# Kernel optimization log

Measured on AMD Instinct MI355X. Metric: run time of the kernel, lower is better.

## Reference

```python
import jax, jax.numpy as jnp
import numpy as np

# ---- config mirroring init kwargs ----
D_MODEL = 512
NUM_DIRS = 8
QUANTILES = (0.1, 0.5, 0.9)
POLY_ORDER = 2
BETA_INIT = 0.5
HEAD_WIDTH = 16
SOFTSORT_C = 0.5
SOFTSORT_ALPHA = 0.5
FEAT_IN = NUM_DIRS * (len(QUANTILES) + POLY_ORDER + 1)  # 48


def _legendre_basis(T, order, dtype):
    t = jnp.linspace(-1.0, 1.0, T, dtype=dtype)
    P = [jnp.ones_like(t)]
    if order >= 1:
        P.append(t)
    for n in range(1, order):
        P.append(((2 * n + 1) * t * P[n] - n * P[n - 1]) / (n + 1))
    B = jnp.stack(P[:order + 1], axis=0)
    return B / jnp.sqrt(jnp.maximum(jnp.sum(B * B, axis=1, keepdims=True), 1e-6))


def _isotonic_nonincreasing(y):
    #   v_i = min_{s<=i} max_{t>=i} mean(y[s..t])
    T = y.shape[0]
    c = jnp.concatenate([jnp.zeros((1,), y.dtype), jnp.cumsum(y)])
    s_idx = jnp.arange(T)[:, None]
    t_idx = jnp.arange(T)[None, :]
    length = jnp.maximum(t_idx - s_idx + 1, 1).astype(y.dtype)
    A = (c[t_idx + 1] - c[s_idx]) / length                 # mean over [s, t]
    A = jnp.where(t_idx >= s_idx, A, -jnp.inf)
    R = jax.lax.cummax(A, axis=1, reverse=True)            # R[s,i] = max_{t>=i} A[s,t]
    R = jnp.where(s_idx <= t_idx, R, jnp.inf)
    V = jax.lax.cummin(R, axis=0)                          # V[i,i] = min_{s<=i} R[s,i]
    return jnp.diagonal(V)


def _soft_sort_ascending(vals, reg):
    # Blondel et al. fast-soft-sort with L2 regularization.
    # Descending soft-sort: rho/reg - isotonic_nonincreasing(rho/reg - sort_desc(theta))
    # Ascending = -soft_sort_desc(-vals).
    L, T = vals.shape
    theta = -vals
    s = jnp.sort(theta, axis=-1)[:, ::-1]                  # descending
    rho = jnp.arange(T, 0, -1, dtype=vals.dtype) / jnp.asarray(reg, vals.dtype)
    v = jax.vmap(_isotonic_nonincreasing)(rho[None, :] - s)
    return -(rho[None, :] - v)


def setup_inputs() -> dict:
    key = jax.random.key(0)
    ks = jax.random.split(key, 6)
    B, T, N, D = 2, 128, 128, D_MODEL
    x = jax.random.normal(ks[0], (B, T, N, D), dtype=jnp.float32)
    valid_mask = jnp.ones((B, T, N), dtype=jnp.float32)
    # proj: Linear(D, K, bias=False), kaiming-uniform-ish init
    bound = 1.0 / np.sqrt(D)
    W_proj = jax.random.uniform(ks[1], (NUM_DIRS, D), jnp.float32, -bound, bound)
    # additive head: per-feature Linear(1,width) -> GELU -> Linear(width,D,no bias)
    W1 = jax.random.uniform(ks[2], (FEAT_IN, HEAD_WIDTH), jnp.float32, -1.0, 1.0)
    b1 = jax.random.uniform(ks[3], (FEAT_IN, HEAD_WIDTH), jnp.float32, -1.0, 1.0)
    bw = 1.0 / np.sqrt(HEAD_WIDTH)
    W2 = jax.random.uniform(ks[4], (FEAT_IN, HEAD_WIDTH, D_MODEL), jnp.float32, -bw, bw)
    beta = jnp.full((D_MODEL,), BETA_INIT, dtype=jnp.float32)
    return {"x": x, "valid_mask": valid_mask, "W_proj": W_proj,
            "W1": W1, "b1": b1, "W2": W2, "beta": beta}


def reference(x, valid_mask, W_proj, W1, b1, W2, beta):
    B, T, N, D = x.shape
    K = W_proj.shape[0]
    # orthonormalize projection (done in-place under no_grad in torch -> straight-through)
    Q, _ = jnp.linalg.qr(W_proj.T)                          # [D, K]
    W_eff = W_proj + jax.lax.stop_gradient(Q.T - W_proj)
    U = W_eff.T                                             # [D, K]

    v = jnp.einsum('btnd,dk->btnk', x, U) * valid_mask[..., None]
    v_bnkt = jnp.transpose(v, (0, 2, 3, 1))                 # [B, N, K, T]

    reg = max(1e-3, SOFTSORT_C * float(T) ** (-SOFTSORT_ALPHA))
    ss = _soft_sort_ascending(v_bnkt.reshape(-1, T), reg)   # [L, T]

    levels = jnp.asarray(QUANTILES, x.dtype)
    pos = jnp.clip(levels, 0.0, 1.0) * (T - 1)
    lo = jnp.clip(jnp.floor(pos).astype(jnp.int32), 0, T - 1)
    hi = jnp.clip(jnp.ceil(pos).astype(jnp.int32), 0, T - 1)
    w = pos - lo.astype(x.dtype)
    qv = ((1.0 - w) * ss[:, lo] + w * ss[:, hi]).reshape(B, N, K, -1)

    Bmat = _legendre_basis(T, POLY_ORDER, x.dtype)          # [P+1, T]
    coeff = jnp.einsum('bnkt,pt->bnkp', v_bnkt, Bmat)

    feats = jnp.concatenate([qv, coeff], axis=-1).reshape(B, N, -1)  # [B, N, F]
    hmid = jax.nn.gelu(feats[..., None] * W1 + b1, approximate=False)  # [B, N, F, width]
    parts = jnp.einsum('bnfw,fwd->bnfd', hmid, W2)          # [B, N, F, D]
    y = parts.sum(axis=2)                                   # [B, N, D]

    beta_eff = jax.nn.sigmoid(beta)
    y_btnd = jnp.broadcast_to(y[:, None], (B, T, N, D))
    h = x + beta_eff * y_btnd
    vm = valid_mask[..., None]
    h = vm * h + (1.0 - vm) * x

    num = jnp.mean(jnp.sqrt(jnp.sum((beta_eff * y_btnd) ** 2, axis=-1)))
    den = jnp.maximum(jnp.mean(jnp.sqrt(jnp.sum(x * x, axis=-1))), 1e-9)
    r = jax.lax.stop_gradient(num / den)
    # per-feature energy: contributions are constant over T -> factor T inside sqrt
    sq = jnp.sum((beta_eff * parts) ** 2, axis=(1, 3))       # [B, F]
    energy = jnp.sqrt(jnp.asarray(T, x.dtype) * sq)
    r_feat = jax.lax.stop_gradient(jnp.mean(energy, axis=0) / den)
    return h, r, r_feat
```

## Files before the change

### kernel.cpp

```cpp
#include <hip/hip_runtime.h>
#include <hip/hip_bf16.h>
#include <math.h>

#define OFF_FEATS 5504
#define OFF_DENP  17792
#define OFF_NUMP  18816
#define OFF_SQP   19072
#define OFF_V     31360
#define OFF_Y     293504
#define OFF_YP    424576
#define WS_TOTAL  1473152

__device__ __align__(16) float g_ws[WS_TOTAL];

static __device__ __forceinline__ float wred64(float v){
  #pragma unroll
  for (int m = 32; m >= 1; m >>= 1) v += __shfl_xor(v, m, 64);
  return v;
}

__global__ __launch_bounds__(256) void k2_proj(const float* __restrict__ x,
                                               const float* __restrict__ vmask,
                                               const float* __restrict__ Wp){
  int tid = threadIdx.x;
  int l = tid & 63, wv = tid >> 6;
  int g = blockIdx.x*4 + wv;
  __shared__ float denw[4];
  float A[8][8], u[8][8], tau[8];
  #pragma unroll
  for (int c = 0; c < 8; c++)
    #pragma unroll
    for (int p = 0; p < 8; p++)
      A[c][p] = Wp[c*512 + l*8 + p];
  #pragma unroll
  for (int j = 0; j < 8; j++){
    float alpha = __shfl(A[j][j & 7], j >> 3, 64);
    float ssq = 0.0f;
    #pragma unroll
    for (int p = 0; p < 8; p++){
      int row = l*8 + p;
      float v = A[j][p];
      ssq += (row > j) ? v*v : 0.0f;
    }
    ssq = wred64(ssq);
    float tj, scale;
    if (ssq == 0.0f){ tj = 0.0f; scale = 0.0f; }
    else {
      float bta = -copysignf(sqrtf(alpha*alpha + ssq), alpha);
      tj = (bta - alpha)/bta;
      scale = 1.0f/(alpha - bta);
    }
    tau[j] = tj;
    #pragma unroll
    for (int p = 0; p < 8; p++){
      int row = l*8 + p;
      float v = A[j][p]*scale;
      A[j][p] = (row < j) ? 0.0f : (row == j ? 1.0f : v);
    }
    #pragma unroll
    for (int c = j+1; c < 8; c++){
      float d = 0.0f;
      #pragma unroll
      for (int p = 0; p < 8; p++) d += A[c][p]*A[j][p];
      d = wred64(d)*tj;
      #pragma unroll
      for (int p = 0; p < 8; p++) A[c][p] -= d*A[j][p];
    }
  }
  #pragma unroll
  for (int c = 0; c < 8; c++)
    #pragma unroll
    for (int p = 0; p < 8; p++)
      u[c][p] = (l*8 + p == c) ? 1.0f : 0.0f;
  #pragma unroll
  for (int j = 7; j >= 0; j--){
    #pragma unroll
    for (int c = 0; c < 8; c++){
      float d = 0.0f;
      #pragma unroll
      for (int p = 0; p < 8; p++) d += u[c][p]*A[j][p];
      d = wred64(d)*tau[j];
      #pragma unroll
      for (int p = 0; p < 8; p++) u[c][p] -= d*A[j][p];
    }
  }
  int kk = ((l & 1) << 2) | (l & 2) | ((l & 4) >> 2);
  float denpart = 0.0f;
  for (int rr = 0; rr < 8; rr++){
    int row = g*8 + rr;
    const float* xr = x + (size_t)row*512 + l*8;
    float4 xa = *(const float4*)xr;
    float4 xb = *(const float4*)(xr + 4);
    float xe[8] = {xa.x, xa.y, xa.z, xa.w, xb.x, xb.y, xb.z, xb.w};
    float acc[8];
    float sq = 0.0f;
    #pragma unroll
    for (int k = 0; k < 8; k++){
      float a = 0.0f;
      #pragma unroll
      for (int e = 0; e < 8; e++) a += xe[e]*u[k][e];
      acc[k] = a;
    }
    #pragma unroll
    for (int e = 0; e < 8; e++) sq += xe[e]*xe[e];
    if (l & 1){
      float t;
      t=acc[0];acc[0]=acc[4];acc[4]=t;
      t=acc[1];acc[1]=acc[5];acc[5]=t;
      t=acc[2];acc[2]=acc[6];acc[6]=t;
      t=acc[3];acc[3]=acc[7];acc[7]=t;
    }
    acc[0] += __shfl_xor(acc[4], 1, 64);
    acc[1] += __shfl_xor(acc[5], 1, 64);
    acc[2] += __shfl_xor(acc[6], 1, 64);
    acc[3] += __shfl_xor(acc[7], 1, 64);
    if (l & 2){
      float t;
      t=acc[0];acc[0]=acc[2];acc[2]=t;
      t=acc[1];acc[1]=acc[3];acc[3]=t;
    }
    acc[0] += __shfl_xor(acc[2], 2, 64);
    acc[1] += __shfl_xor(acc[3], 2, 64);
    if (l & 4){
      float t=acc[0];acc[0]=acc[1];acc[1]=t;
    }
    acc[0] += __shfl_xor(acc[1], 4, 64);
    acc[0] += __shfl_xor(acc[0], 8, 64);
    acc[0] += __shfl_xor(acc[0], 16, 64);
    acc[0] += __shfl_xor(acc[0], 32, 64);
    sq = wred64(sq);
    float vm = vmask[row];
    if (l < 8){
      int b = row >> 14, t = (row >> 7) & 127, n = row & 127;
      int bn = b*128 + n;
      g_ws[OFF_V + bn*1024 + kk*128 + t] = acc[0]*vm;
    }
    if (l == 0) denpart += sqrtf(sq);
  }
  if (l == 0) denw[wv] = denpart;
  __syncthreads();
  if (tid == 0) g_ws[OFF_DENP + blockIdx.x] = denw[0]+denw[1]+denw[2]+denw[3];
}

__global__ __launch_bounds__(256) void k3_sortfeat(){
  int tid = threadIdx.x;
  int l = tid & 63, wv = tid >> 6;
  int rho = blockIdx.x*4 + wv;
  __shared__ float orig[4][128], srt[4][128], Bl[384];
  __shared__ float pS[4][128];
  __shared__ int   pC[4][128];
  __shared__ float nrmS[2];
  if (tid < 128){
    float t = -1.0f + 2.0f*(float)tid/127.0f;
    Bl[128+tid] = t;
    Bl[256+tid] = 0.5f*(3.0f*t*t - 1.0f);
  }
  const float* vr = g_ws + OFF_V + rho*128;
  orig[wv][2*l]   = vr[2*l];
  orig[wv][2*l+1] = vr[2*l+1];
  srt[wv][2*l] = 0.0f; srt[wv][2*l+1] = 0.0f;
  __syncthreads();
  if (tid < 64){
    float a = Bl[128+tid]*Bl[128+tid] + Bl[192+tid]*Bl[192+tid];
    float b = Bl[256+tid]*Bl[256+tid] + Bl[320+tid]*Bl[320+tid];
    a = wred64(a); b = wred64(b);
    if (tid == 0){
      nrmS[0] = sqrtf(fmaxf(a, 1e-6f));
      nrmS[1] = sqrtf(fmaxf(b, 1e-6f));
    }
  }
  __syncthreads();
  if (tid < 128){
    Bl[tid] = 0.08838834764831845f;
    Bl[128+tid] /= nrmS[0];
    Bl[256+tid] /= nrmS[1];
  }
  __syncthreads();
  float c0, c1, c2;
  {
    float a = orig[wv][2*l], b = orig[wv][2*l+1];
    c0 = a*Bl[2*l]       + b*Bl[2*l+1];
    c1 = a*Bl[128+2*l]   + b*Bl[128+2*l+1];
    c2 = a*Bl[256+2*l]   + b*Bl[256+2*l+1];
  }
  c0 = wred64(c0); c1 = wred64(c1); c2 = wred64(c2);
  float e0 = orig[wv][2*l], e1 = orig[wv][2*l+1];
  int r0 = 0, r1 = 0;
  #pragma unroll 4
  for (int j = 0; j < 128; j++){
    float vj = orig[wv][j];
    r0 += (vj < e0) || (vj == e0 && j < 2*l);
    r1 += (vj < e1) || (vj == e1 && j < 2*l+1);
  }
  srt[wv][r0] = e0;
  srt[wv][r1] = e1;
  __syncthreads();
  const float rinv = 22.627416997969522f;
  bool v0 = (srt[wv][2*l+1] - srt[wv][2*l] > rinv);
  bool v1 = (2*l + 2 < 128) ? (srt[wv][2*l+2] - srt[wv][2*l+1] > rinv) : false;
  if (__any(v0 || v1)){
    if (l == 0){
      int top = -1;
      for (int i = 0; i < 128; i++){
        float y = (float)(128 - i)*rinv + srt[wv][i];
        top++; pS[wv][top] = y; pC[wv][top] = 1;
        while (top > 0 &&
               pS[wv][top]*(float)pC[wv][top-1] > pS[wv][top-1]*(float)pC[wv][top]){
          pS[wv][top-1] += pS[wv][top];
          pC[wv][top-1] += pC[wv][top];
          top--;
        }
      }
      int i = 0;
      for (int blk = 0; blk <= top; blk++){
        float m = pS[wv][blk]/(float)pC[wv][blk];
        for (int c = 0; c < pC[wv][blk]; c++){
          srt[wv][i] = m - (float)(128 - i)*rinv;
          i++;
        }
      }
    }
  }
  if (l == 0){
    int bn = rho >> 3, k = rho & 7;
    float* fb = g_ws + OFF_FEATS + bn*48 + k*6;
    float w0 = 0.1f*127.0f - 12.0f;
    float w1 = 0.5f*127.0f - 63.0f;
    float w2 = 0.9f*127.0f - 114.0f;
    fb[0] = (1.0f - w0)*srt[wv][12]  + w0*srt[wv][13];
    fb[1] = (1.0f - w1)*srt[wv][63]  + w1*srt[wv][64];
    fb[2] = (1.0f - w2)*srt[wv][114] + w2*srt[wv][115];
    fb[3] = c0; fb[4] = c1; fb[5] = c2;
  }
}

__global__ __launch_bounds__(512) void k4a_head(const float* __restrict__ W1,
                                                const float* __restrict__ b1,
                                                const float* __restrict__ W2,
                                                const float* __restrict__ beta){
  int blk = blockIdx.x;
  int s   = blk & 7;
  int bnp = blk >> 3;
  int bn0 = bnp*2, bn1 = bn0 + 1;
  int tid = threadIdx.x;
  int l = tid & 63, wv = tid >> 6;
  __shared__ float hl0[96], hl1[96];
  __shared__ float sq[8][12];
  if (tid < 192){
    int which = tid >= 96;
    int i = which ? tid - 96 : tid;
    int f = s*6 + (i >> 4);
    int k = f*16 + (i & 15);
    int bn = which ? bn1 : bn0;
    float a = g_ws[OFF_FEATS + bn*48 + f]*W1[k] + b1[k];
    float g = 0.5f*a*(1.0f + erff(a*0.70710678118654752f));
    if (which) hl1[i] = g; else hl0[i] = g;
  }
  __syncthreads();
  int d = tid;
  float be = 1.0f/(1.0f + expf(-beta[d]));
  float b2 = be*be;
  float y0 = 0.0f, y1 = 0.0f;
  float ev[12];
  const float* w2base = W2 + (size_t)(s*96)*512 + d;
  #pragma unroll
  for (int fl_ = 0; fl_ < 6; fl_++){
    float p0 = 0.0f, p1 = 0.0f;
    #pragma unroll
    for (int w = 0; w < 16; w++){
      float w2 = w2base[(size_t)(fl_*16 + w)*512];
      p0 += hl0[fl_*16 + w]*w2;
      p1 += hl1[fl_*16 + w]*w2;
    }
    y0 += p0; y1 += p1;
    ev[fl_*2]     = p0*p0*b2;
    ev[fl_*2 + 1] = p1*p1*b2;
  }
  g_ws[OFF_YP + (size_t)(bn0*8 + s)*512 + d] = y0;
  g_ws[OFF_YP + (size_t)(bn1*8 + s)*512 + d] = y1;
  int kk = ((l & 1) << 2) | (l & 2) | ((l & 4) >> 2);
  {
    float a0=ev[0],a1=ev[1],a2=ev[2],a3=ev[3],a4=ev[4],a5=ev[5],a6=ev[6],a7=ev[7];
    if (l & 1){ float t; t=a0;a0=a4;a4=t; t=a1;a1=a5;a5=t; t=a2;a2=a6;a6=t; t=a3;a3=a7;a7=t; }
    a0 += __shfl_xor(a4,1,64); a1 += __shfl_xor(a5,1,64);
    a2 += __shfl_xor(a6,1,64); a3 += __shfl_xor(a7,1,64);
    if (l & 2){ float t; t=a0;a0=a2;a2=t; t=a1;a1=a3;a3=t; }
    a0 += __shfl_xor(a2,2,64); a1 += __shfl_xor(a3,2,64);
    if (l & 4){ float t=a0;a0=a1;a1=t; }
    a0 += __shfl_xor(a1,4,64);
    a0 += __shfl_xor(a0,8,64); a0 += __shfl_xor(a0,16,64); a0 += __shfl_xor(a0,32,64);
    if (l < 8) sq[wv][kk] = a0;
  }
  {
    float a0=ev[8],a1=ev[9],a2=ev[10],a3=ev[11],a4=0,a5=0,a6=0,a7=0;
    if (l & 1){ float t; t=a0;a0=a4;a4=t; t=a1;a1=a5;a5=t; t=a2;a2=a6;a6=t; t=a3;a3=a7;a7=t; }
    a0 += __shfl_xor(a4,1,64); a1 += __shfl_xor(a5,1,64);
    a2 += __shfl_xor(a6,1,64); a3 += __shfl_xor(a7,1,64);
    if (l & 2){ float t; t=a0;a0=a2;a2=t; t=a1;a1=a3;a3=t; }
    a0 += __shfl_xor(a2,2,64); a1 += __shfl_xor(a3,2,64);
    if (l & 4){ float t=a0;a0=a1;a1=t; }
    a0 += __shfl_xor(a1,4,64);
    a0 += __shfl_xor(a0,8,64); a0 += __shfl_xor(a0,16,64); a0 += __shfl_xor(a0,32,64);
    if (l < 8 && kk < 4) sq[wv][8 + kk] = a0;
  }
  __syncthreads();
  if (tid < 12){
    float t = 0.0f;
    #pragma unroll
    for (int w = 0; w < 8; w++) t += sq[w][tid];
    int fl_ = tid >> 1, which = tid & 1;
    int bn = which ? bn1 : bn0;
    g_ws[OFF_SQP + bn*48 + s*6 + fl_] = t;
  }
}

__global__ __launch_bounds__(512) void k4b_red(const float* __restrict__ beta){
  int bn = blockIdx.x;
  int tid = threadIdx.x;
  int l = tid & 63, wv = tid >> 6;
  __shared__ float nw[8];
  float y = 0.0f;
  #pragma unroll
  for (int s = 0; s < 8; s++) y += g_ws[OFF_YP + (size_t)(bn*8 + s)*512 + tid];
  g_ws[OFF_Y + bn*512 + tid] = y;
  float be = 1.0f/(1.0f + expf(-beta[tid]));
  float by = be*y;
  float ns = wred64(by*by);
  if (l == 0) nw[wv] = ns;
  __syncthreads();
  if (tid == 0){
    float s = nw[0]+nw[1]+nw[2]+nw[3]+nw[4]+nw[5]+nw[6]+nw[7];
    g_ws[OFF_NUMP + bn] = sqrtf(s);
  }
}

__global__ __launch_bounds__(256) void k7_out(const float* __restrict__ x,
                                              const float* __restrict__ vmask,
                                              const float* __restrict__ beta,
                                              float* __restrict__ outt){
  if (blockIdx.x == 16384){
    __shared__ float red[256];
    __shared__ float en[96];
    __shared__ float scal[2];
    int tid = threadIdx.x;
    float dp = 0.0f;
    for (int i = tid; i < 1024; i += 256) dp += g_ws[OFF_DENP + i];
    red[tid] = dp; __syncthreads();
    for (int s = 128; s > 0; s >>= 1){
      if (tid < s) red[tid] += red[tid + s];
      __syncthreads();
    }
    if (tid == 0) scal[0] = fmaxf(red[0]/32768.0f, 1e-9f);
    __syncthreads();
    red[tid] = g_ws[OFF_NUMP + tid];
    __syncthreads();
    for (int s = 128; s > 0; s >>= 1){
      if (tid < s) red[tid] += red[tid + s];
      __syncthreads();
    }
    if (tid == 0) scal[1] = red[0]/256.0f;
    __syncthreads();
    float den = scal[0];
    if (tid < 96){
      int b = tid/48, f = tid%48;
      float s = 0.0f;
      for (int j = 0; j < 128; j++) s += g_ws[OFF_SQP + (b*128 + j)*48 + f];
      en[tid] = sqrtf(128.0f*s);
    }
    __syncthreads();
    if (tid == 0) outt[16777216] = scal[1]/den;
    if (tid < 48) outt[16777217 + tid] = 0.5f*(en[tid] + en[48 + tid])/den;
    return;
  }
  int q = blockIdx.x*256 + threadIdx.x;
  size_t fl = (size_t)q*4;
  int d = (int)(fl & 511);
  int row = (int)(fl >> 9);
  int b = row >> 14, n = row & 127;
  int bn = b*128 + n;
  float vm = vmask[row];
  float4 xv = *(const float4*)(x + fl);
  float4 yv = *(const float4*)(g_ws + OFF_Y + bn*512 + d);
  float4 bt = *(const float4*)(beta + d);
  float4 bv;
  bv.x = 1.0f/(1.0f + expf(-bt.x));
  bv.y = 1.0f/(1.0f + expf(-bt.y));
  bv.z = 1.0f/(1.0f + expf(-bt.z));
  bv.w = 1.0f/(1.0f + expf(-bt.w));
  float4 o;
  o.x = xv.x + vm*bv.x*yv.x;
  o.y = xv.y + vm*bv.y*yv.y;
  o.z = xv.z + vm*bv.z*yv.z;
  o.w = xv.w + vm*bv.w*yv.w;
  *(float4*)(outt + fl) = o;
}

extern "C" void kernel_launch(void* const* d_in, const int* in_sizes, int n_in,
                              void* d_out, int out_size, void* d_ws, size_t ws_size,
                              hipStream_t stream){
  (void)out_size; (void)d_ws; (void)ws_size;
  const float *x=nullptr,*vm=nullptr,*Wp=nullptr,*W1=nullptr,*b1=nullptr,*W2=nullptr,*beta=nullptr;
  for (int i = 0; i < n_in; i++){
    int s = in_sizes[i];
    const float* p = (const float*)d_in[i];
    if      (s == 16777216) x = p;
    else if (s == 32768)    vm = p;
    else if (s == 4096)     Wp = p;
    else if (s == 393216)   W2 = p;
    else if (s == 512)      beta = p;
    else if (s == 768)      { if (!W1) W1 = p; else b1 = p; }
  }
  float* out = (float*)d_out;

  k2_proj<<<1024, 256, 0, stream>>>(x, vm, Wp);
  k3_sortfeat<<<512, 256, 0, stream>>>();
  k4a_head<<<1024, 512, 0, stream>>>(W1, b1, W2, beta);
  k4b_red<<<256, 512, 0, stream>>>(beta);
  k7_out<<<16385, 256, 0, stream>>>(x, vm, beta, out);
}
```

Before: 100.3 us.

## Hoist Householder QR of projection into a single prep kernel and batch reductions

Moves the per-wave Householder orthogonalization of W_proj, which every one of the 4096 waves recomputed redundantly, into a one-block prep kernel that writes Q to workspace. k2_proj then just loads Q. The cross-lane reductions are also restructured so that eight rows' partial sums are reduced together, and all 64 lanes write one output each instead of eight lanes per row. This adds a tiny extra launch and a serial dependency in exchange for removing a large amount of redundant shuffle-heavy work.

```diff
diff --git a/kernel.cpp b/kernel.cpp
--- a/kernel.cpp
+++ b/kernel.cpp
@@ -2,6 +2,7 @@
 #include <hip/hip_bf16.h>
 #include <math.h>
 
+#define OFF_U     0
 #define OFF_FEATS 5504
 #define OFF_DENP  17792
 #define OFF_NUMP  18816
@@ -19,28 +20,23 @@
   return v;
 }
 
-__global__ __launch_bounds__(256) void k2_proj(const float* __restrict__ x,
-                                               const float* __restrict__ vmask,
-                                               const float* __restrict__ Wp){
-  int tid = threadIdx.x;
-  int l = tid & 63, wv = tid >> 6;
-  int g = blockIdx.x*4 + wv;
-  __shared__ float denw[4];
-  float A[8][8], u[8][8], tau[8];
+__global__ __launch_bounds__(64) void k1_prep(const float* __restrict__ Wp){
+  int l = threadIdx.x;
+  float A[8][8], Q[8][8], tau[8];
   #pragma unroll
   for (int c = 0; c < 8; c++)
     #pragma unroll
     for (int p = 0; p < 8; p++)
-      A[c][p] = Wp[c*512 + l*8 + p];
+      A[c][p] = Wp[c*512 + p*64 + l];
   #pragma unroll
   for (int j = 0; j < 8; j++){
-    float alpha = __shfl(A[j][j & 7], j >> 3, 64);
+    float alpha = __shfl(A[j][0], j, 64);
     float ssq = 0.0f;
     #pragma unroll
     for (int p = 0; p < 8; p++){
-      int row = l*8 + p;
+      bool live = (p > 0) || (l > j);
       float v = A[j][p];
-      ssq += (row > j) ? v*v : 0.0f;
+      ssq += live ? v*v : 0.0f;
     }
     ssq = wred64(ssq);
     float tj, scale;
@@ -53,7 +49,7 @@
     tau[j] = tj;
     #pragma unroll
     for (int p = 0; p < 8; p++){
-      int row = l*8 + p;
+      int row = p*64 + l;
       float v = A[j][p]*scale;
       A[j][p] = (row < j) ? 0.0f : (row == j ? 1.0f : v);
     }
@@ -71,21 +67,41 @@
   for (int c = 0; c < 8; c++)
     #pragma unroll
     for (int p = 0; p < 8; p++)
-      u[c][p] = (l*8 + p == c) ? 1.0f : 0.0f;
+      Q[c][p] = (p == 0 && l == c) ? 1.0f : 0.0f;
   #pragma unroll
   for (int j = 7; j >= 0; j--){
     #pragma unroll
     for (int c = 0; c < 8; c++){
       float d = 0.0f;
       #pragma unroll
-      for (int p = 0; p < 8; p++) d += u[c][p]*A[j][p];
+      for (int p = 0; p < 8; p++) d += Q[c][p]*A[j][p];
       d = wred64(d)*tau[j];
       #pragma unroll
-      for (int p = 0; p < 8; p++) u[c][p] -= d*A[j][p];
-    }
-  }
+      for (int p = 0; p < 8; p++) Q[c][p] -= d*A[j][p];
+    }
+  }
+  #pragma unroll
+  for (int c = 0; c < 8; c++)
+    #pragma unroll
+    for (int p = 0; p < 8; p++)
+      g_ws[OFF_U + c*512 + p*64 + l] = Q[c][p];
+}
+
+__global__ __launch_bounds__(256) void k2_proj(const float* __restrict__ x,
+                                               const float* __restrict__ vmask){
+  int tid = threadIdx.x;
+  int l = tid & 63, wv = tid >> 6;
+  int g = blockIdx.x*4 + wv;
+  __shared__ float denw[4];
+  float u[8][8];
+  #pragma unroll
+  for (int k = 0; k < 8; k++)
+    #pragma unroll
+    for (int e = 0; e < 8; e++)
+      u[k][e] = g_ws[OFF_U + k*512 + l*8 + e];
   int kk = ((l & 1) << 2) | (l & 2) | ((l & 4) >> 2);
-  float denpart = 0.0f;
+  float pacc[8], psq[8];
+  #pragma unroll
   for (int rr = 0; rr < 8; rr++){
     int row = g*8 + rr;
     const float* xr = x + (size_t)row*512 + l*8;
@@ -125,19 +141,57 @@
       float t=acc[0];acc[0]=acc[1];acc[1]=t;
     }
     acc[0] += __shfl_xor(acc[1], 4, 64);
-    acc[0] += __shfl_xor(acc[0], 8, 64);
-    acc[0] += __shfl_xor(acc[0], 16, 64);
-    acc[0] += __shfl_xor(acc[0], 32, 64);
-    sq = wred64(sq);
-    float vm = vmask[row];
-    if (l < 8){
-      int b = row >> 14, t = (row >> 7) & 127, n = row & 127;
-      int bn = b*128 + n;
-      g_ws[OFF_V + bn*1024 + kk*128 + t] = acc[0]*vm;
-    }
-    if (l == 0) denpart += sqrtf(sq);
-  }
-  if (l == 0) denw[wv] = denpart;
+    pacc[rr] = acc[0];
+    psq[rr]  = sq;
+  }
+  #pragma unroll
+  for (int rr = 0; rr < 8; rr++){
+    pacc[rr] += __shfl_xor(pacc[rr],  8, 64);
+    pacc[rr] += __shfl_xor(pacc[rr], 16, 64);
+    pacc[rr] += __shfl_xor(pacc[rr], 32, 64);
+  }
+  if (l & 1){
+    float t;
+    t=psq[0];psq[0]=psq[4];psq[4]=t;
+    t=psq[1];psq[1]=psq[5];psq[5]=t;
+    t=psq[2];psq[2]=psq[6];psq[6]=t;
+    t=psq[3];psq[3]=psq[7];psq[7]=t;
+  }
+  psq[0] += __shfl_xor(psq[4], 1, 64);
+  psq[1] += __shfl_xor(psq[5], 1, 64);
+  psq[2] += __shfl_xor(psq[6], 1, 64);
+  psq[3] += __shfl_xor(psq[7], 1, 64);
+  if (l & 2){
+    float t;
+    t=psq[0];psq[0]=psq[2];psq[2]=t;
+    t=psq[1];psq[1]=psq[3];psq[3]=t;
+  }
+  psq[0] += __shfl_xor(psq[2], 2, 64);
+  psq[1] += __shfl_xor(psq[3], 2, 64);
+  if (l & 4){
+    float t=psq[0];psq[0]=psq[1];psq[1]=t;
+  }
+  psq[0] += __shfl_xor(psq[1], 4, 64);
+  psq[0] += __shfl_xor(psq[0], 8, 64);
+  psq[0] += __shfl_xor(psq[0], 16, 64);
+  psq[0] += __shfl_xor(psq[0], 32, 64);
+  float dsq = sqrtf(psq[0]);
+  dsq += __shfl_xor(dsq, 1, 64);
+  dsq += __shfl_xor(dsq, 2, 64);
+  dsq += __shfl_xor(dsq, 4, 64);
+  float c0 = (l & 32) ? pacc[4] : pacc[0];
+  float c1 = (l & 32) ? pacc[5] : pacc[1];
+  float c2 = (l & 32) ? pacc[6] : pacc[2];
+  float c3 = (l & 32) ? pacc[7] : pacc[3];
+  float d0 = (l & 16) ? c2 : c0;
+  float d1 = (l & 16) ? c3 : c1;
+  float val = (l & 8) ? d1 : d0;
+  int rowl = g*8 + (l >> 3);
+  float vm = vmask[rowl];
+  int b = rowl >> 14, t = (rowl >> 7) & 127, n = rowl & 127;
+  int bn = b*128 + n;
+  g_ws[OFF_V + bn*1024 + kk*128 + t] = val*vm;
+  if (l == 0) denw[wv] = dsq;
   __syncthreads();
   if (tid == 0) g_ws[OFF_DENP + blockIdx.x] = denw[0]+denw[1]+denw[2]+denw[3];
 }
@@ -412,7 +466,8 @@
   }
   float* out = (float*)d_out;
 
-  k2_proj<<<1024, 256, 0, stream>>>(x, vm, Wp);
+  k1_prep<<<1, 64, 0, stream>>>(Wp);
+  k2_proj<<<1024, 256, 0, stream>>>(x, vm);
   k3_sortfeat<<<512, 256, 0, stream>>>();
   k4a_head<<<1024, 512, 0, stream>>>(W1, b1, W2, beta);
   k4b_red<<<256, 512, 0, stream>>>(beta);
```

New measurement: 87.44 us. -12.8%, faster.
